# Optimization experiments

Measured on AMD Instinct MI355X. Metric: run time of the kernel, lower is better.

## Reference

```python
import jax, jax.numpy as jnp
import numpy as np

B, S, D, H = 8, 4096, 1024, 16
DH = D // H  # head size = 64


def setup_inputs() -> dict:
    key = jax.random.key(0)
    ks = jax.random.split(key, 9)
    scale = 1.0 / np.sqrt(D)
    x = jax.random.normal(ks[0], (B, S, D), dtype=jnp.float32)
    wq = jax.random.normal(ks[1], (D, D), dtype=jnp.float32) * scale
    bq = jnp.zeros((D,), dtype=jnp.float32)
    wk = jax.random.normal(ks[2], (D, D), dtype=jnp.float32) * scale
    bk = jnp.zeros((D,), dtype=jnp.float32)
    wv = jax.random.normal(ks[3], (D, D), dtype=jnp.float32) * scale
    bv = jnp.zeros((D,), dtype=jnp.float32)
    wo = jax.random.normal(ks[4], (D, D), dtype=jnp.float32) * scale
    bo = jnp.zeros((D,), dtype=jnp.float32)
    return {"x": x, "wq": wq, "bq": bq, "wk": wk, "bk": bk,
            "wv": wv, "bv": bv, "wo": wo, "bo": bo}


def reference(x, wq, bq, wk, bk, wv, bv, wo, bo):
    b, s, d = x.shape
    # torch Linear: y = x @ W^T + b
    q = (x @ wq.T + bq).reshape(b, s, H, DH)
    k = (x @ wk.T + bk).reshape(b, s, H, DH)
    v = (x @ wv.T + bv).reshape(b, s, H, DH)
    # NOTE: original transpose_for_scores only reshapes (no permute), so
    # matmul(q, k.transpose(-1,-2)) contracts over head_size and the softmax
    # runs over the HEAD axis per token: scores shape [B, S, H, H].
    scores = jnp.einsum('bshd,bsgd->bshg', q, k) / jnp.sqrt(jnp.float32(DH))
    probs = jax.nn.softmax(scores, axis=-1)
    ctx = jnp.einsum('bshg,bsgd->bshd', probs, v).reshape(b, s, d)
    return ctx @ wo.T + bo
```

## Files before the change

### kernel.cpp

```cpp
#include <hip/hip_runtime.h>
#include <hip/hip_bf16.h>


#define DEV static __device__ __forceinline__

typedef __attribute__((ext_vector_type(8))) _Float16 fp16x8;
typedef __attribute__((ext_vector_type(4))) float f32x4;

DEV unsigned short f2h(float f) {
    union { _Float16 h; unsigned short u; } c;
    c.h = (_Float16)f;
    return c.u;
}

DEV void gl_lds16(const void* g, void* l) {
    __builtin_amdgcn_global_load_lds(
        (const __attribute__((address_space(1))) unsigned int*)g,
        (__attribute__((address_space(3))) unsigned int*)l, 16, 0, 0);
}

__global__ __launch_bounds__(256) void k_convert(
    const float* __restrict__ x,
    const float* __restrict__ wq, const float* __restrict__ wk,
    const float* __restrict__ wv, const float* __restrict__ wo,
    const float* __restrict__ bq, const float* __restrict__ bk,
    const float* __restrict__ bv,
    unsigned short* __restrict__ Xb, unsigned short* __restrict__ Wb,
    unsigned short* __restrict__ Wob, float* __restrict__ biasc)
{
    const int NX = 33554432 / 4;
    const int NW = 3145728 / 4;
    const int NO = 1048576 / 4;
    const int NB = 3072 / 4;
    const int total = NX + NW + NO + NB;
    for (int c = blockIdx.x * blockDim.x + threadIdx.x; c < total;
         c += gridDim.x * blockDim.x) {
        if (c < NX) {
            float4 v = ((const float4*)x)[c];
            uint2 u;
            u.x = f2h(v.x) | ((unsigned int)f2h(v.y) << 16);
            u.y = f2h(v.z) | ((unsigned int)f2h(v.w) << 16);
            ((uint2*)Xb)[c] = u;
        } else if (c < NX + NW) {
            int e = c - NX;
            const float* w = (e < 262144) ? wq : (e < 524288) ? wk : wv;
            int off = e & 262143;
            float4 v = ((const float4*)w)[off];
            uint2 u;
            u.x = f2h(v.x) | ((unsigned int)f2h(v.y) << 16);
            u.y = f2h(v.z) | ((unsigned int)f2h(v.w) << 16);
            ((uint2*)Wb)[e] = u;
        } else if (c < NX + NW + NO) {
            int e = c - NX - NW;
            float4 v = ((const float4*)wo)[e];
            uint2 u;
            u.x = f2h(v.x) | ((unsigned int)f2h(v.y) << 16);
            u.y = f2h(v.z) | ((unsigned int)f2h(v.w) << 16);
            ((uint2*)Wob)[e] = u;
        } else {
            int e = c - NX - NW - NO;
            const float* b = (e < 256) ? bq : (e < 512) ? bk : bv;
            int off = e & 255;
            ((float4*)biasc)[e] = ((const float4*)b)[off];
        }
    }
}

template <bool OUT_F16>
__global__ __launch_bounds__(256) void k_gemm_bt(
    const unsigned short* __restrict__ A,
    const unsigned short* __restrict__ B,
    const float* __restrict__ bias,
    unsigned short* __restrict__ Ch,
    float* __restrict__ Cf,
    int ldc)
{
    __shared__ __align__(16) unsigned short As[128 * 32];
    __shared__ __align__(16) unsigned short Bs[128 * 32];

    const int tid  = threadIdx.x;
    const int lane = tid & 63;
    const int w    = tid >> 6;
    const int wr   = w >> 1, wc = w & 1;
    const int quad = lane >> 4;
    const int lr   = lane & 15;

    const int m0 = blockIdx.y * 128;
    const int n0 = blockIdx.x * 128;

    f32x4 acc[4][4];
#pragma unroll
    for (int i = 0; i < 4; ++i)
#pragma unroll
        for (int j = 0; j < 4; ++j) {
            f32x4 z = {0.f, 0.f, 0.f, 0.f};
            acc[i][j] = z;
        }

    const int id0 = tid, id1 = tid + 256;
    const int ar0 = id0 >> 2, ac0 = (id0 & 3) * 8;
    const int ar1 = id1 >> 2, ac1 = (id1 & 3) * 8;
    const unsigned short* Arow0 = A + (size_t)(m0 + ar0) * 1024 + ac0;
    const unsigned short* Arow1 = A + (size_t)(m0 + ar1) * 1024 + ac1;
    const unsigned short* Brow0 = B + (size_t)(n0 + ar0) * 1024 + ac0;
    const unsigned short* Brow1 = B + (size_t)(n0 + ar1) * 1024 + ac1;

    for (int k0 = 0; k0 < 1024; k0 += 32) {
        __syncthreads();
        gl_lds16(Arow0 + k0, (char*)As + id0 * 16);
        gl_lds16(Arow1 + k0, (char*)As + id1 * 16);
        gl_lds16(Brow0 + k0, (char*)Bs + id0 * 16);
        gl_lds16(Brow1 + k0, (char*)Bs + id1 * 16);
        asm volatile("s_waitcnt vmcnt(0)" ::: "memory");
        __syncthreads();

        fp16x8 a[4], b[4];
#pragma unroll
        for (int i = 0; i < 4; ++i)
            a[i] = *(const fp16x8*)(const void*)&As[(wr * 64 + i * 16 + lr) * 32 + quad * 8];
#pragma unroll
        for (int j = 0; j < 4; ++j)
            b[j] = *(const fp16x8*)(const void*)&Bs[(wc * 64 + j * 16 + lr) * 32 + quad * 8];
#pragma unroll
        for (int i = 0; i < 4; ++i)
#pragma unroll
            for (int j = 0; j < 4; ++j)
                acc[i][j] = __builtin_amdgcn_mfma_f32_16x16x32_f16(a[i], b[j], acc[i][j], 0, 0, 0);
    }

    float bj[4];
#pragma unroll
    for (int j = 0; j < 4; ++j) bj[j] = bias[n0 + wc * 64 + j * 16 + lr];
#pragma unroll
    for (int i = 0; i < 4; ++i) {
        const int mrow = m0 + wr * 64 + i * 16 + quad * 4;
#pragma unroll
        for (int j = 0; j < 4; ++j) {
            const int ncol = n0 + wc * 64 + j * 16 + lr;
#pragma unroll
            for (int r = 0; r < 4; ++r) {
                float v = acc[i][j][r] + bj[j];
                if (OUT_F16)
                    Ch[(size_t)(mrow + r) * ldc + ncol] = f2h(v);
                else
                    Cf[(size_t)(mrow + r) * ldc + ncol] = v;
            }
        }
    }
}

__global__ __launch_bounds__(256) void k_attn(
    const unsigned short* __restrict__ qkv,
    unsigned short* __restrict__ Ctx)
{
    __shared__ __align__(16) unsigned short sqk[4][32 * 72];
    __shared__ __align__(16) unsigned short svt[4][64 * 24];
    __shared__ __align__(16) unsigned short spp[4][16 * 24];

    const int tid  = threadIdx.x;
    const int wv   = tid >> 6;
    const int l    = tid & 63;
    const int t    = blockIdx.x * 4 + wv;
    const unsigned short* tok = qkv + (size_t)t * 3072;

    unsigned short* qk = sqk[wv];
    unsigned short* vt = svt[wv];
    unsigned short* pp = spp[wv];

    const int quad = l >> 4;
    const int lr   = l & 15;
    const int row8 = l >> 3;
    const int col8 = (l & 7) * 8;

#pragma unroll
    for (int i = 0; i < 4; ++i) {
        const int row = i * 8 + row8;
        uint4 u = *(const uint4*)(tok + i * 512 + l * 8);
        *(uint4*)&qk[row * 72 + col8] = u;
    }
#pragma unroll
    for (int i = 0; i < 2; ++i) {
        const int g = i * 8 + row8;
        uint4 u = *(const uint4*)(tok + 2048 + i * 512 + l * 8);
        const unsigned short* hu = (const unsigned short*)&u;
#pragma unroll
        for (int c = 0; c < 8; ++c)
            vt[(col8 + c) * 24 + g] = hu[c];
    }
    asm volatile("s_waitcnt lgkmcnt(0)" ::: "memory");

    f32x4 s = {0.f, 0.f, 0.f, 0.f};
#pragma unroll
    for (int ks = 0; ks < 2; ++ks) {
        fp16x8 aq = *(const fp16x8*)(const void*)&qk[lr * 72 + ks * 32 + quad * 8];
        fp16x8 bk = *(const fp16x8*)(const void*)&qk[(16 + lr) * 72 + ks * 32 + quad * 8];
        s = __builtin_amdgcn_mfma_f32_16x16x32_f16(aq, bk, s, 0, 0, 0);
    }

#pragma unroll
    for (int r = 0; r < 4; ++r) {
        float sv = s[r] * 0.125f;
        float m = sv;
        m = fmaxf(m, __shfl_xor(m, 1, 64));
        m = fmaxf(m, __shfl_xor(m, 2, 64));
        m = fmaxf(m, __shfl_xor(m, 4, 64));
        m = fmaxf(m, __shfl_xor(m, 8, 64));
        float e = __expf(sv - m);
        float su = e;
        su += __shfl_xor(su, 1, 64);
        su += __shfl_xor(su, 2, 64);
        su += __shfl_xor(su, 4, 64);
        su += __shfl_xor(su, 8, 64);
        float p = e * __builtin_amdgcn_rcpf(su);
        pp[(quad * 4 + r) * 24 + lr] = f2h(p);
    }
    asm volatile("s_waitcnt lgkmcnt(0)" ::: "memory");

    fp16x8 pa;
    if (quad < 2) {
        pa = *(const fp16x8*)(const void*)&pp[lr * 24 + quad * 8];
    } else {
#pragma unroll
        for (int j = 0; j < 8; ++j) pa[j] = (_Float16)0.f;
    }

    f32x4 c[4];
#pragma unroll
    for (int nb = 0; nb < 4; ++nb) {
        fp16x8 bv;
        if (quad < 2) {
            bv = *(const fp16x8*)(const void*)&vt[(nb * 16 + lr) * 24 + quad * 8];
        } else {
#pragma unroll
            for (int j = 0; j < 8; ++j) bv[j] = (_Float16)0.f;
        }
        f32x4 z = {0.f, 0.f, 0.f, 0.f};
        c[nb] = __builtin_amdgcn_mfma_f32_16x16x32_f16(pa, bv, z, 0, 0, 0);
    }
    asm volatile("s_waitcnt lgkmcnt(0)" ::: "memory");

#pragma unroll
    for (int nb = 0; nb < 4; ++nb)
#pragma unroll
        for (int r = 0; r < 4; ++r)
            qk[(quad * 4 + r) * 72 + nb * 16 + lr] = f2h(c[nb][r]);
    asm volatile("s_waitcnt lgkmcnt(0)" ::: "memory");

    unsigned short* dst = Ctx + (size_t)t * 1024;
#pragma unroll
    for (int i = 0; i < 2; ++i) {
        const int row = i * 8 + row8;
        uint4 u = *(const uint4*)&qk[row * 72 + col8];
        *(uint4*)(dst + row * 64 + col8) = u;
    }
}

extern "C" void kernel_launch(void* const* d_in, const int* in_sizes, int n_in,
                              void* d_out, int out_size, void* d_ws, size_t ws_size,
                              hipStream_t stream)
{
    (void)in_sizes; (void)n_in; (void)out_size;

    const float* x  = (const float*)d_in[0];
    const float* wq = (const float*)d_in[1];
    const float* bq = (const float*)d_in[2];
    const float* wk = (const float*)d_in[3];
    const float* bk = (const float*)d_in[4];
    const float* wv = (const float*)d_in[5];
    const float* bv = (const float*)d_in[6];
    const float* wo = (const float*)d_in[7];
    const float* bo = (const float*)d_in[8];

    if (ws_size < 276836352ull) return;

    char* ws = (char*)d_ws;
    unsigned short* QKV  = (unsigned short*)(ws);
    unsigned short* Xb   = (unsigned short*)(ws + 201326592);
    unsigned short* Wb   = (unsigned short*)(ws + 268435456);
    unsigned short* Wob  = (unsigned short*)(ws + 274726912);
    float*          bqkv = (float*)(ws + 276824064);
    unsigned short* Ctx  = Xb;

    k_convert<<<2048, 256, 0, stream>>>(x, wq, wk, wv, wo, bq, bk, bv,
                                        Xb, Wb, Wob, bqkv);
    k_gemm_bt<true><<<dim3(24, 256), 256, 0, stream>>>(
        Xb, Wb, bqkv, QKV, nullptr, 3072);
    k_attn<<<8192, 256, 0, stream>>>(QKV, Ctx);
    k_gemm_bt<false><<<dim3(8, 256), 256, 0, stream>>>(
        Ctx, Wob, bo, nullptr, (float*)d_out, 1024);
}
```

Before: 637.8 us.

## Replace GEMM with 256x256 double-buffered, swizzled-LDS pipelined kernel

```diff
diff --git a/kernel.cpp b/kernel.cpp
--- a/kernel.cpp
+++ b/kernel.cpp
@@ -66,74 +66,140 @@
     }
 }
 
+template <int MODE>
+DEV void g256_tile(const unsigned short* __restrict__ Ac,
+                   const unsigned short* __restrict__ Bc,
+                   unsigned short* As_stg, unsigned short* Bs_stg,
+                   const unsigned short* gA, const unsigned short* gB,
+                   int tid, int rA, int rB, int c0, int c1,
+                   f32x4 (&acc)[8][4])
+{
+    fp16x8 a0[8], b0[4];
+#pragma unroll
+    for (int i = 0; i < 8; ++i)
+        a0[i] = *(const fp16x8*)(const void*)&Ac[rA + i * 1024 + c0];
+#pragma unroll
+    for (int j = 0; j < 4; ++j)
+        b0[j] = *(const fp16x8*)(const void*)&Bc[rB + j * 1024 + c0];
+#pragma unroll
+    for (int i = 0; i < 8; ++i)
+#pragma unroll
+        for (int j = 0; j < 4; ++j)
+            acc[i][j] = __builtin_amdgcn_mfma_f32_16x16x32_f16(a0[i], b0[j], acc[i][j], 0, 0, 0);
+
+    fp16x8 a1[8], b1[4];
+#pragma unroll
+    for (int i = 0; i < 8; ++i)
+        a1[i] = *(const fp16x8*)(const void*)&Ac[rA + i * 1024 + c1];
+#pragma unroll
+    for (int j = 0; j < 4; ++j)
+        b1[j] = *(const fp16x8*)(const void*)&Bc[rB + j * 1024 + c1];
+
+    asm volatile("s_waitcnt lgkmcnt(0)" ::: "memory");
+    __builtin_amdgcn_sched_barrier(0);
+    __builtin_amdgcn_s_barrier();
+    asm volatile("" ::: "memory");
+
+    if (MODE == 0) {
+#pragma unroll
+        for (int s = 0; s < 4; ++s) {
+            gl_lds16(gA + (size_t)s * 65536, (char*)As_stg + (tid + s * 512) * 16);
+            gl_lds16(gB + (size_t)s * 65536, (char*)Bs_stg + (tid + s * 512) * 16);
+        }
+        __builtin_amdgcn_sched_barrier(0);
+    }
+
+    __builtin_amdgcn_s_setprio(1);
+#pragma unroll
+    for (int i = 0; i < 8; ++i)
+#pragma unroll
+        for (int j = 0; j < 4; ++j)
+            acc[i][j] = __builtin_amdgcn_mfma_f32_16x16x32_f16(a1[i], b1[j], acc[i][j], 0, 0, 0);
+    __builtin_amdgcn_s_setprio(0);
+
+    if (MODE == 0) asm volatile("s_waitcnt vmcnt(8)" ::: "memory");
+    if (MODE == 1) asm volatile("s_waitcnt vmcnt(0)" ::: "memory");
+    if (MODE != 2) {
+        __builtin_amdgcn_s_barrier();
+        asm volatile("" ::: "memory");
+    }
+}
+
 template <bool OUT_F16>
-__global__ __launch_bounds__(256) void k_gemm_bt(
+__global__ __launch_bounds__(512, 2) void k_gemm256(
     const unsigned short* __restrict__ A,
     const unsigned short* __restrict__ B,
     const float* __restrict__ bias,
     unsigned short* __restrict__ Ch,
     float* __restrict__ Cf,
-    int ldc)
-{
-    __shared__ __align__(16) unsigned short As[128 * 32];
-    __shared__ __align__(16) unsigned short Bs[128 * 32];
+    int ldc, int nbx)
+{
+    __shared__ __align__(16) unsigned short As[2][256 * 64];
+    __shared__ __align__(16) unsigned short Bs[2][256 * 64];
 
     const int tid  = threadIdx.x;
     const int lane = tid & 63;
     const int w    = tid >> 6;
-    const int wr   = w >> 1, wc = w & 1;
+    const int wr   = w >> 2, wc = w & 3;
     const int quad = lane >> 4;
     const int lr   = lane & 15;
 
-    const int m0 = blockIdx.y * 128;
-    const int n0 = blockIdx.x * 128;
-
-    f32x4 acc[4][4];
-#pragma unroll
-    for (int i = 0; i < 4; ++i)
+    const int cpx = gridDim.x >> 3;
+    const int id  = (blockIdx.x & 7) * cpx + (blockIdx.x >> 3);
+    const int by  = id / nbx, bx = id - by * nbx;
+    const int m0  = by * 256, n0 = bx * 256;
+
+    const int srow = tid >> 3;
+    const int kk   = (((tid & 7) ^ (srow & 7)) << 3);
+    const unsigned short* gAp = A + (size_t)(m0 + srow) * 1024 + kk;
+    const unsigned short* gBp = B + (size_t)(n0 + srow) * 1024 + kk;
+
+    const int swz = (lr & 7) << 3;
+    const int c0  = (quad * 8) ^ swz;
+    const int c1  = c0 ^ 32;
+    const int rA  = (wr * 128 + lr) * 64;
+    const int rB  = (wc * 64 + lr) * 64;
+
+    f32x4 acc[8][4];
+#pragma unroll
+    for (int i = 0; i < 8; ++i)
 #pragma unroll
         for (int j = 0; j < 4; ++j) {
             f32x4 z = {0.f, 0.f, 0.f, 0.f};
             acc[i][j] = z;
         }
 
-    const int id0 = tid, id1 = tid + 256;
-    const int ar0 = id0 >> 2, ac0 = (id0 & 3) * 8;
-    const int ar1 = id1 >> 2, ac1 = (id1 & 3) * 8;
-    const unsigned short* Arow0 = A + (size_t)(m0 + ar0) * 1024 + ac0;
-    const unsigned short* Arow1 = A + (size_t)(m0 + ar1) * 1024 + ac1;
-    const unsigned short* Brow0 = B + (size_t)(n0 + ar0) * 1024 + ac0;
-    const unsigned short* Brow1 = B + (size_t)(n0 + ar1) * 1024 + ac1;
-
-    for (int k0 = 0; k0 < 1024; k0 += 32) {
-        __syncthreads();
-        gl_lds16(Arow0 + k0, (char*)As + id0 * 16);
-        gl_lds16(Arow1 + k0, (char*)As + id1 * 16);
-        gl_lds16(Brow0 + k0, (char*)Bs + id0 * 16);
-        gl_lds16(Brow1 + k0, (char*)Bs + id1 * 16);
-        asm volatile("s_waitcnt vmcnt(0)" ::: "memory");
-        __syncthreads();
-
-        fp16x8 a[4], b[4];
-#pragma unroll
-        for (int i = 0; i < 4; ++i)
-            a[i] = *(const fp16x8*)(const void*)&As[(wr * 64 + i * 16 + lr) * 32 + quad * 8];
-#pragma unroll
-        for (int j = 0; j < 4; ++j)
-            b[j] = *(const fp16x8*)(const void*)&Bs[(wc * 64 + j * 16 + lr) * 32 + quad * 8];
-#pragma unroll
-        for (int i = 0; i < 4; ++i)
-#pragma unroll
-            for (int j = 0; j < 4; ++j)
-                acc[i][j] = __builtin_amdgcn_mfma_f32_16x16x32_f16(a[i], b[j], acc[i][j], 0, 0, 0);
-    }
+#pragma unroll
+    for (int s = 0; s < 4; ++s) {
+        gl_lds16(gAp + (size_t)s * 65536, (char*)As[0] + (tid + s * 512) * 16);
+        gl_lds16(gBp + (size_t)s * 65536, (char*)Bs[0] + (tid + s * 512) * 16);
+    }
+#pragma unroll
+    for (int s = 0; s < 4; ++s) {
+        gl_lds16(gAp + (size_t)s * 65536 + 64, (char*)As[1] + (tid + s * 512) * 16);
+        gl_lds16(gBp + (size_t)s * 65536 + 64, (char*)Bs[1] + (tid + s * 512) * 16);
+    }
+    asm volatile("s_waitcnt vmcnt(8)" ::: "memory");
+    __builtin_amdgcn_s_barrier();
+    asm volatile("" ::: "memory");
+
+    const unsigned short* gAt = gAp + 128;
+    const unsigned short* gBt = gBp + 128;
+    for (int t = 0; t < 14; t += 2) {
+        g256_tile<0>(As[0], Bs[0], As[0], Bs[0], gAt, gBt, tid, rA, rB, c0, c1, acc);
+        gAt += 64; gBt += 64;
+        g256_tile<0>(As[1], Bs[1], As[1], Bs[1], gAt, gBt, tid, rA, rB, c0, c1, acc);
+        gAt += 64; gBt += 64;
+    }
+    g256_tile<1>(As[0], Bs[0], As[0], Bs[0], gAt, gBt, tid, rA, rB, c0, c1, acc);
+    g256_tile<2>(As[1], Bs[1], As[1], Bs[1], gAt, gBt, tid, rA, rB, c0, c1, acc);
 
     float bj[4];
 #pragma unroll
     for (int j = 0; j < 4; ++j) bj[j] = bias[n0 + wc * 64 + j * 16 + lr];
 #pragma unroll
-    for (int i = 0; i < 4; ++i) {
-        const int mrow = m0 + wr * 64 + i * 16 + quad * 4;
+    for (int i = 0; i < 8; ++i) {
+        const int mrow = m0 + wr * 128 + i * 16 + quad * 4;
 #pragma unroll
         for (int j = 0; j < 4; ++j) {
             const int ncol = n0 + wc * 64 + j * 16 + lr;
@@ -283,9 +349,9 @@
 
     k_convert<<<2048, 256, 0, stream>>>(x, wq, wk, wv, wo, bq, bk, bv,
                                         Xb, Wb, Wob, bqkv);
-    k_gemm_bt<true><<<dim3(24, 256), 256, 0, stream>>>(
-        Xb, Wb, bqkv, QKV, nullptr, 3072);
+    k_gemm256<true><<<1536, 512, 0, stream>>>(
+        Xb, Wb, bqkv, QKV, nullptr, 3072, 12);
     k_attn<<<8192, 256, 0, stream>>>(QKV, Ctx);
-    k_gemm_bt<false><<<dim3(8, 256), 256, 0, stream>>>(
-        Ctx, Wob, bo, nullptr, (float*)d_out, 1024);
-}
+    k_gemm256<false><<<512, 512, 0, stream>>>(
+        Ctx, Wob, bo, nullptr, (float*)d_out, 1024, 4);
+}
```

Result: faster. 592.4 us (-7.1%).
